# Kernel tuning notes

Measured on AMD Instinct MI355X. Metric: run time of the kernel, lower is better.

Reference implementation:

```python
import jax, jax.numpy as jnp
import numpy as np

B, S, F, DV, H, DH, L = 32, 600, 9, 1024, 16, 64, 2


def setup_inputs() -> dict:
    key = jax.random.key(0)
    ks = jax.random.split(key, 24)
    w = lambda k, shape, s=0.05: jax.random.normal(k, shape, dtype=jnp.float32) * s
    return {
        "x": w(ks[0], (B, S, F), 1.0),
        "enc_in_W": w(ks[1], (F, DV)), "enc_in_b": w(ks[2], (DV,)),
        "Wq": w(ks[3], (L, H, DV, DH)), "bq": w(ks[4], (L, H, DH)),
        "Wk": w(ks[5], (L, H, DV, DH)), "bk": w(ks[6], (L, H, DH)),
        "Wv": w(ks[7], (L, H, DV, DH)), "bv": w(ks[8], (L, H, DH)),
        "Wo": w(ks[9], (L, DV, DV)), "bo": w(ks[10], (L, DV)),
        "W1": w(ks[11], (L, DV, DV)), "b1": w(ks[12], (L, DV)),
        "W2": w(ks[13], (L, DV, DV)), "b2": w(ks[14], (L, DV)),
        "ln1_w": jnp.ones((L, DV)), "ln1_b": jnp.zeros((L, DV)),
        "ln2_w": jnp.ones((L, DV)), "ln2_b": jnp.zeros((L, DV)),
        "out_W": w(ks[15], (DV, F)), "out_b": w(ks[16], (F,)),
    }


def _layernorm(v, g, b):
    mu = v.mean(-1, keepdims=True)
    var = v.var(-1, keepdims=True)  # biased, matches torch LayerNorm
    return (v - mu) / jnp.sqrt(var + 1e-5) * g + b


def reference(x, enc_in_W, enc_in_b, Wq, bq, Wk, bk, Wv, bv, Wo, bo,
              W1, b1, W2, b2, ln1_w, ln1_b, ln2_w, ln2_b, out_W, out_b):
    # enc_input_fc; pe skipped (code checks pe_mode == 'stardard', never true)
    h = x @ enc_in_W + enc_in_b  # [B,S,DV]
    scale = 1.0 / jnp.sqrt(jnp.float32(DH))
    for l in range(L):
        q = jnp.einsum('bsd,hdk->bhsk', h, Wq[l]) + bq[l][None, :, None, :]
        k = jnp.einsum('bsd,hdk->bhsk', h, Wk[l]) + bk[l][None, :, None, :]
        v = jnp.einsum('bsd,hdk->bhsk', h, Wv[l]) + bv[l][None, :, None, :]
        attn = jax.nn.softmax(jnp.einsum('bhsk,bhtk->bhst', q, k) * scale, axis=-1)
        ctx = jnp.einsum('bhst,bhtk->bhsk', attn, v)  # [B,H,S,DH]
        # torch: stack(heads, dim=-1) -> [B,S,DH,H], then flatten(start_dim=2)
        a = ctx.transpose(0, 2, 3, 1).reshape(B, S, DH * H)
        attn_out = a @ Wo[l] + bo[l]
        x1 = _layernorm(h + attn_out, ln1_w[l], ln1_b[l])
        ff = jax.nn.elu(x1 @ W2[l] + b2[l]) @ W1[l] + b1[l]  # fc1(elu(fc2(x1)))
        h = _layernorm(x1 + ff, ln2_w[l], ln2_b[l])
    out = h @ out_W + out_b  # [B,S,F]; in_seq_len == out_seq_len -> no out_seq_fc
    return out
```

## Files before the change

### kernel.cpp

```cpp
#include <hip/hip_runtime.h>

typedef unsigned short u16;
typedef unsigned int u32;
typedef __attribute__((ext_vector_type(8))) short shortx8;
typedef __attribute__((ext_vector_type(4))) float floatx4;
typedef __attribute__((ext_vector_type(4))) u32 uintx4;
typedef __attribute__((ext_vector_type(2))) u32 uintx2;

#define AS1 __attribute__((address_space(1)))
#define AS3 __attribute__((address_space(3)))

__device__ __forceinline__ float bf2f(u16 u) {
  return __builtin_bit_cast(float, ((u32)u) << 16);
}
__device__ __forceinline__ u16 f2bf(float f) {
  u32 i = __builtin_bit_cast(u32, f);
  u32 r = (i + 0x7fffu + ((i >> 16) & 1u)) >> 16;
  return (u16)r;
}

__launch_bounds__(256)
__global__ void pack_qkv_t(const float* __restrict__ W, u16* __restrict__ dst) {
  __shared__ u16 T[64][72];
  const int kt = blockIdx.x, y = blockIdx.y;
  const int l = y >> 4, h = y & 15;
  const int t = threadIdx.x;
  const int rr = t >> 2, cq = (t & 3) * 16;
  const float* src = W + ((size_t)y * 1024 + kt * 64 + rr) * 64 + cq;
#pragma unroll
  for (int e4 = 0; e4 < 4; ++e4) {
    float4 f = *(const float4*)(src + e4 * 4);
    T[cq + e4 * 4 + 0][rr] = f2bf(f.x);
    T[cq + e4 * 4 + 1][rr] = f2bf(f.y);
    T[cq + e4 * 4 + 2][rr] = f2bf(f.z);
    T[cq + e4 * 4 + 3][rr] = f2bf(f.w);
  }
  __syncthreads();
  const int dd = t >> 2, kq = (t & 3) * 16;
  u16* drow = dst + (size_t)l * 3145728 + ((size_t)h * 64 + dd) * 1024 + kt * 64 + kq;
  *(uintx4*)(drow) = *(const uintx4*)&T[dd][kq];
  *(uintx4*)(drow + 8) = *(const uintx4*)&T[dd][kq + 8];
}

__launch_bounds__(256)
__global__ void pack_sq_t(const float* __restrict__ W, u16* __restrict__ dst) {
  __shared__ u16 T[64][72];
  const int ct = blockIdx.x & 15, rt = blockIdx.x >> 4, l = blockIdx.y;
  const int t = threadIdx.x;
  const int rr = t >> 2, cq = (t & 3) * 16;
  const float* src = W + (size_t)l * 1048576 + (size_t)(rt * 64 + rr) * 1024 + ct * 64 + cq;
#pragma unroll
  for (int e4 = 0; e4 < 4; ++e4) {
    float4 f = *(const float4*)(src + e4 * 4);
    T[cq + e4 * 4 + 0][rr] = f2bf(f.x);
    T[cq + e4 * 4 + 1][rr] = f2bf(f.y);
    T[cq + e4 * 4 + 2][rr] = f2bf(f.z);
    T[cq + e4 * 4 + 3][rr] = f2bf(f.w);
  }
  __syncthreads();
  const int cc = t >> 2, rq = (t & 3) * 16;
  u16* drow = dst + (size_t)l * 1048576 + (size_t)(ct * 64 + cc) * 1024 + rt * 64 + rq;
  *(uintx4*)(drow) = *(const uintx4*)&T[cc][rq];
  *(uintx4*)(drow + 8) = *(const uintx4*)&T[cc][rq + 8];
}

__launch_bounds__(256)
__global__ void pack_wo_t(const float* __restrict__ W, u16* __restrict__ dst) {
  __shared__ u16 T[64][72];
  const int rt = blockIdx.x >> 4, nt = blockIdx.x & 15, l = blockIdx.y;
  const int t = threadIdx.x;
  const int rr = t >> 2, cq = (t & 3) * 16;
  const float* src = W + (size_t)l * 1048576 + (size_t)(rt * 64 + rr) * 1024 + nt * 64 + cq;
#pragma unroll
  for (int e4 = 0; e4 < 4; ++e4) {
    float4 f = *(const float4*)(src + e4 * 4);
    T[cq + e4 * 4 + 0][rr] = f2bf(f.x);
    T[cq + e4 * 4 + 1][rr] = f2bf(f.y);
    T[cq + e4 * 4 + 2][rr] = f2bf(f.z);
    T[cq + e4 * 4 + 3][rr] = f2bf(f.w);
  }
  __syncthreads();
  const int hh = t & 15;
#pragma unroll
  for (int pass = 0; pass < 4; ++pass) {
    const int nl = pass * 16 + (t >> 4);
    uintx2 pk;
    u16 v0 = T[nl][0 * 16 + hh], v1 = T[nl][1 * 16 + hh];
    u16 v2 = T[nl][2 * 16 + hh], v3 = T[nl][3 * 16 + hh];
    pk[0] = (u32)v0 | ((u32)v1 << 16);
    pk[1] = (u32)v2 | ((u32)v3 << 16);
    *(uintx2*)&dst[(size_t)l * 1048576 + (size_t)(nt * 64 + nl) * 1024 + hh * 64 + rt * 4] = pk;
  }
}

__launch_bounds__(256)
__global__ void pack_bias(const float* __restrict__ bq, const float* __restrict__ bk,
                          const float* __restrict__ bv, float* __restrict__ bias) {
  const int i = blockIdx.x * 256 + threadIdx.x;
  const int l = i / 3072, n = i % 3072;
  const int which = n >> 10, nn = n & 1023;
  const float* s = (which == 0) ? bq : (which == 1) ? bk : bv;
  bias[i] = s[l * 1024 + nn];
}

__launch_bounds__(256)
__global__ void enc_kernel(const float* __restrict__ x, const float* __restrict__ W,
                           const float* __restrict__ bias, u16* __restrict__ h) {
  const size_t i = (size_t)blockIdx.x * 256 + threadIdx.x;
  const int m = (int)(i >> 10), n = (int)(i & 1023);
  const float* xr = x + (size_t)m * 9;
  float acc = bias[n];
#pragma unroll
  for (int f = 0; f < 9; ++f) acc += xr[f] * W[f * 1024 + n];
  h[i] = f2bf(acc);
}

template <int EPI>
__launch_bounds__(512)
__global__ void gemm_bt_wide(const u16* __restrict__ A, int lda,
                             const u16* __restrict__ Bt,
                             const float* __restrict__ bias,
                             const u16* __restrict__ R, int ldr,
                             u16* __restrict__ C, int ldc) {
  constexpr int K = 1024;
  __shared__ u16 As[128 * 64];
  __shared__ u16 Bs[256 * 64];
  const int tid = threadIdx.x;
  const int lane = tid & 63;
  const int w = tid >> 6;
  const int wr = w >> 2, wc = w & 3;
  const int m0 = blockIdx.y * 128, n0 = blockIdx.x * 256;

  floatx4 acc[4][4];
#pragma unroll
  for (int i = 0; i < 4; ++i)
#pragma unroll
    for (int j = 0; j < 4; ++j) acc[i][j] = (floatx4){0.f, 0.f, 0.f, 0.f};

  const u16* Ab = A + (size_t)m0 * lda;
  const u16* Bb = Bt + (size_t)n0 * K;

  for (int k0 = 0; k0 < K; k0 += 64) {
#pragma unroll
    for (int p = 0; p < 2; ++p) {
      const int o = p * 8192 + tid * 16;
      const int row = o >> 7;
      const int ke = (o & 127) >> 1;
      __builtin_amdgcn_global_load_lds((const AS1 void*)(Ab + (size_t)row * lda + (k0 + ke)),
                                       (AS3 void*)((char*)As + o), 16, 0, 0);
    }
#pragma unroll
    for (int p = 0; p < 4; ++p) {
      const int o = p * 8192 + tid * 16;
      const int row = o >> 7;
      const int ke = (o & 127) >> 1;
      __builtin_amdgcn_global_load_lds((const AS1 void*)(Bb + (size_t)row * K + (k0 + ke)),
                                       (AS3 void*)((char*)Bs + o), 16, 0, 0);
    }
    __syncthreads();
#pragma unroll
    for (int ks = 0; ks < 2; ++ks) {
      shortx8 af[4], bfr[4];
#pragma unroll
      for (int i = 0; i < 4; ++i) {
        const int ar = wr * 64 + i * 16 + (lane & 15);
        af[i] = *(const shortx8*)&As[ar * 64 + ks * 32 + (lane >> 4) * 8];
        const int br = wc * 64 + i * 16 + (lane & 15);
        bfr[i] = *(const shortx8*)&Bs[br * 64 + ks * 32 + (lane >> 4) * 8];
      }
#pragma unroll
      for (int i = 0; i < 4; ++i)
#pragma unroll
        for (int j = 0; j < 4; ++j)
          acc[i][j] = __builtin_amdgcn_mfma_f32_16x16x32_bf16(af[i], bfr[j], acc[i][j], 0, 0, 0);
    }
    __syncthreads();
  }

  const int lr = (lane >> 4) * 4, lc = lane & 15;
#pragma unroll
  for (int i = 0; i < 4; ++i) {
#pragma unroll
    for (int j = 0; j < 4; ++j) {
      const int col = n0 + wc * 64 + j * 16 + lc;
      const float bv = bias[col];
#pragma unroll
      for (int r = 0; r < 4; ++r) {
        const int row = m0 + wr * 64 + i * 16 + lr + r;
        float v = acc[i][j][r] + bv;
        if (EPI == 1) v += bf2f(R[(size_t)row * ldr + col]);
        if (EPI == 2) v = v > 0.f ? v : expm1f(v);
        C[(size_t)row * ldc + col] = f2bf(v);
      }
    }
  }
}

__launch_bounds__(256)
__global__ void attn_mfma(const u16* __restrict__ qkv, u16* __restrict__ aout) {
  const int qt = blockIdx.x, bh = blockIdx.y;
  const int b = bh >> 4, h = bh & 15;
  const int tid = threadIdx.x, lane = tid & 63, w = tid >> 6;
  const int g = lane >> 4, lq = lane & 15;

  __shared__ u16 K_ld[128 * 72];
  __shared__ u16 Vt[64 * 136];
  __shared__ u16 P_ld[4][16 * 136];

  const size_t bbase = (size_t)b * 600 * 3072;
  const int q0 = qt * 128 + w * 32;

  shortx8 aq[2][2];
#pragma unroll
  for (int sub = 0; sub < 2; ++sub) {
    const int s = q0 + sub * 16 + lq;
    if (s < 600) {
      const u16* qp = qkv + bbase + (size_t)s * 3072 + h * 64 + g * 8;
      aq[sub][0] = *(const shortx8*)qp;
      aq[sub][1] = *(const shortx8*)(qp + 32);
    } else {
      aq[sub][0] = (shortx8){0, 0, 0, 0, 0, 0, 0, 0};
      aq[sub][1] = (shortx8){0, 0, 0, 0, 0, 0, 0, 0};
    }
  }

  floatx4 Oa[2][4];
  float m[2][4], l[2][4];
#pragma unroll
  for (int sub = 0; sub < 2; ++sub) {
#pragma unroll
    for (int db = 0; db < 4; ++db) Oa[sub][db] = (floatx4){0.f, 0.f, 0.f, 0.f};
#pragma unroll
    for (int r = 0; r < 4; ++r) { m[sub][r] = -1e30f; l[sub][r] = 0.f; }
  }

  for (int ch = 0; ch < 5; ++ch) {
    const int t0 = ch * 128;
    __syncthreads();
    {
      const int tloc = tid >> 1, dhalf = (tid & 1) * 32;
      const int tg = t0 + tloc;
      if (tg < 600) {
        const u16* kp = qkv + bbase + (size_t)tg * 3072 + 1024 + h * 64 + dhalf;
        const u16* vp = kp + 1024;
#pragma unroll
        for (int c = 0; c < 4; ++c)
          *(uintx4*)&K_ld[tloc * 72 + dhalf + c * 8] = *(const uintx4*)(kp + c * 8);
#pragma unroll
        for (int c = 0; c < 4; ++c) {
          shortx8 vv = *(const shortx8*)(vp + c * 8);
#pragma unroll
          for (int e = 0; e < 8; ++e)
            Vt[(dhalf + c * 8 + e) * 136 + tloc] = (u16)vv[e];
        }
      } else {
        const uintx4 z4 = (uintx4){0, 0, 0, 0};
#pragma unroll
        for (int c = 0; c < 4; ++c)
          *(uintx4*)&K_ld[tloc * 72 + dhalf + c * 8] = z4;
#pragma unroll
        for (int c = 0; c < 4; ++c)
#pragma unroll
          for (int e = 0; e < 8; ++e)
            Vt[(dhalf + c * 8 + e) * 136 + tloc] = 0;
      }
    }
    __syncthreads();

#pragma unroll
    for (int sub = 0; sub < 2; ++sub) {
      floatx4 S[8];
      __builtin_amdgcn_s_setprio(1);
#pragma unroll
      for (int jb = 0; jb < 8; ++jb) {
        S[jb] = (floatx4){0.f, 0.f, 0.f, 0.f};
#pragma unroll
        for (int ks = 0; ks < 2; ++ks) {
          shortx8 bk = *(const shortx8*)&K_ld[(jb * 16 + lq) * 72 + ks * 32 + g * 8];
          S[jb] = __builtin_amdgcn_mfma_f32_16x16x32_bf16(aq[sub][ks], bk, S[jb], 0, 0, 0);
        }
      }
      __builtin_amdgcn_s_setprio(0);
      if (ch == 4) {
#pragma unroll
        for (int jb = 0; jb < 8; ++jb) {
          const bool ok = (t0 + jb * 16 + lq) < 600;
#pragma unroll
          for (int r = 0; r < 4; ++r) S[jb][r] = ok ? S[jb][r] * 0.125f : -1e30f;
        }
      } else {
#pragma unroll
        for (int jb = 0; jb < 8; ++jb)
#pragma unroll
          for (int r = 0; r < 4; ++r) S[jb][r] *= 0.125f;
      }

      float vmax[4];
      bool need = false;
#pragma unroll
      for (int r = 0; r < 4; ++r) {
        float v = S[0][r];
#pragma unroll
        for (int jb = 1; jb < 8; ++jb) v = fmaxf(v, S[jb][r]);
        v = fmaxf(v, __shfl_xor(v, 1));
        v = fmaxf(v, __shfl_xor(v, 2));
        v = fmaxf(v, __shfl_xor(v, 4));
        v = fmaxf(v, __shfl_xor(v, 8));
        vmax[r] = v;
        need |= (v > m[sub][r] + 8.0f);
      }
      if (__any(need ? 1 : 0)) {
#pragma unroll
        for (int r = 0; r < 4; ++r) {
          const float mn = fmaxf(m[sub][r], vmax[r]);
          const float sc = __expf(m[sub][r] - mn);
          m[sub][r] = mn;
          l[sub][r] *= sc;
#pragma unroll
          for (int db = 0; db < 4; ++db) Oa[sub][db][r] *= sc;
        }
      }

      float sums[4] = {0.f, 0.f, 0.f, 0.f};
#pragma unroll
      for (int jb = 0; jb < 8; ++jb)
#pragma unroll
        for (int r = 0; r < 4; ++r) {
          const float p = __expf(S[jb][r] - m[sub][r]);
          sums[r] += p;
          P_ld[w][(g * 4 + r) * 136 + jb * 16 + lq] = f2bf(p);
        }
#pragma unroll
      for (int r = 0; r < 4; ++r) {
        float v = sums[r];
        v += __shfl_xor(v, 1);
        v += __shfl_xor(v, 2);
        v += __shfl_xor(v, 4);
        v += __shfl_xor(v, 8);
        l[sub][r] += v;
      }

      __builtin_amdgcn_s_setprio(1);
#pragma unroll
      for (int ks = 0; ks < 4; ++ks) {
        shortx8 ap = *(const shortx8*)&P_ld[w][lq * 136 + ks * 32 + g * 8];
#pragma unroll
        for (int db = 0; db < 4; ++db) {
          shortx8 bv = *(const shortx8*)&Vt[(db * 16 + lq) * 136 + ks * 32 + g * 8];
          Oa[sub][db] = __builtin_amdgcn_mfma_f32_16x16x32_bf16(ap, bv, Oa[sub][db], 0, 0, 0);
        }
      }
      __builtin_amdgcn_s_setprio(0);
    }
  }

#pragma unroll
  for (int sub = 0; sub < 2; ++sub) {
#pragma unroll
    for (int r = 0; r < 4; ++r) {
      const int sg = q0 + sub * 16 + g * 4 + r;
      if (sg < 600) {
        const float inv = 1.f / l[sub][r];
        u16* orow = aout + ((size_t)(b * 600 + sg)) * 1024 + h * 64;
#pragma unroll
        for (int db = 0; db < 4; ++db)
          orow[db * 16 + lq] = f2bf(Oa[sub][db][r] * inv);
      }
    }
  }
}

__launch_bounds__(256)
__global__ void ln_kernel(const u16* __restrict__ y, int ldy,
                          const float* __restrict__ g, const float* __restrict__ be,
                          u16* __restrict__ o, int ldo) {
  const int row = blockIdx.x, tid = threadIdx.x;
  const int lane = tid & 63, wv = tid >> 6;
  const u16* yr = y + (size_t)row * ldy;
  const int c = tid * 4;
  const uintx2 yv = *(const uintx2*)&yr[c];
  float v0 = bf2f((u16)(yv[0] & 0xffffu)), v1 = bf2f((u16)(yv[0] >> 16));
  float v2 = bf2f((u16)(yv[1] & 0xffffu)), v3 = bf2f((u16)(yv[1] >> 16));
  float s = v0 + v1 + v2 + v3;
  float q = v0 * v0 + v1 * v1 + v2 * v2 + v3 * v3;
#pragma unroll
  for (int m = 32; m; m >>= 1) {
    s += __shfl_xor(s, m);
    q += __shfl_xor(q, m);
  }
  __shared__ float red[2][4];
  if (lane == 0) {
    red[0][wv] = s;
    red[1][wv] = q;
  }
  __syncthreads();
  s = red[0][0] + red[0][1] + red[0][2] + red[0][3];
  q = red[1][0] + red[1][1] + red[1][2] + red[1][3];
  const float mu = s * (1.f / 1024.f);
  const float var = q * (1.f / 1024.f) - mu * mu;
  const float rstd = rsqrtf(var + 1e-5f);
  const float4 gv = *(const float4*)&g[c];
  const float4 bev = *(const float4*)&be[c];
  const float o0 = (v0 - mu) * rstd * gv.x + bev.x;
  const float o1 = (v1 - mu) * rstd * gv.y + bev.y;
  const float o2 = (v2 - mu) * rstd * gv.z + bev.z;
  const float o3 = (v3 - mu) * rstd * gv.w + bev.w;
  uintx2 ov;
  ov[0] = (u32)f2bf(o0) | ((u32)f2bf(o1) << 16);
  ov[1] = (u32)f2bf(o2) | ((u32)f2bf(o3) << 16);
  *(uintx2*)&o[(size_t)row * ldo + c] = ov;
}

__launch_bounds__(256)
__global__ void out_kernel(const u16* __restrict__ h, const float* __restrict__ W,
                           const float* __restrict__ bias, float* __restrict__ out) {
  const int m = blockIdx.x * 4 + (threadIdx.x >> 6);
  const int lane = threadIdx.x & 63;
  float acc[9];
#pragma unroll
  for (int f = 0; f < 9; ++f) acc[f] = 0.f;
  const u16* hr = h + (size_t)m * 1024;
#pragma unroll 4
  for (int j = 0; j < 16; ++j) {
    const int k = lane + j * 64;
    const float hv = bf2f(hr[k]);
    const float* wr = W + (size_t)k * 9;
#pragma unroll
    for (int f = 0; f < 9; ++f) acc[f] += hv * wr[f];
  }
#pragma unroll
  for (int f = 0; f < 9; ++f)
#pragma unroll
    for (int mm = 32; mm; mm >>= 1) acc[f] += __shfl_xor(acc[f], mm);
  if (lane < 9) out[(size_t)m * 9 + lane] = acc[lane] + bias[lane];
}

extern "C" void kernel_launch(void* const* d_in, const int* in_sizes, int n_in,
                              void* d_out, int out_size, void* d_ws, size_t ws_size,
                              hipStream_t stream) {
  (void)in_sizes; (void)n_in; (void)out_size; (void)ws_size;
  const float* x     = (const float*)d_in[0];
  const float* encW  = (const float*)d_in[1];
  const float* encB  = (const float*)d_in[2];
  const float* Wq    = (const float*)d_in[3];
  const float* bq    = (const float*)d_in[4];
  const float* Wk    = (const float*)d_in[5];
  const float* bk    = (const float*)d_in[6];
  const float* Wv    = (const float*)d_in[7];
  const float* bv    = (const float*)d_in[8];
  const float* Wo    = (const float*)d_in[9];
  const float* bo    = (const float*)d_in[10];
  const float* W1    = (const float*)d_in[11];
  const float* b1    = (const float*)d_in[12];
  const float* W2    = (const float*)d_in[13];
  const float* b2    = (const float*)d_in[14];
  const float* ln1w  = (const float*)d_in[15];
  const float* ln1b  = (const float*)d_in[16];
  const float* ln2w  = (const float*)d_in[17];
  const float* ln2b  = (const float*)d_in[18];
  const float* outW  = (const float*)d_in[19];
  const float* outB  = (const float*)d_in[20];
  float* out = (float*)d_out;

  char* ws = (char*)d_ws;
  size_t off = 0;
  auto alloc = [&](size_t bytes) -> void* {
    void* p = ws + off;
    off += (bytes + 255) & ~(size_t)255;
    return p;
  };
  u16* h    = (u16*)alloc(19660800ull * 2);
  u16* qkv  = (u16*)alloc(58982400ull * 2);
  u16* abuf = (u16*)alloc(19660800ull * 2);
  u16* Bqkv = (u16*)alloc(6291456ull * 2);
  u16* Bwo  = (u16*)alloc(2097152ull * 2);
  u16* Bw1  = (u16*)alloc(2097152ull * 2);
  u16* Bw2  = (u16*)alloc(2097152ull * 2);
  float* bqkv = (float*)alloc(6144ull * 4);
  u16* ybuf = qkv;
  u16* x1   = qkv + 1024;
  u16* mid  = qkv + 2048;
  u16* y2   = abuf;

  pack_qkv_t<<<dim3(16, 32), 256, 0, stream>>>(Wq, Bqkv);
  pack_qkv_t<<<dim3(16, 32), 256, 0, stream>>>(Wk, Bqkv + 1048576);
  pack_qkv_t<<<dim3(16, 32), 256, 0, stream>>>(Wv, Bqkv + 2097152);
  pack_wo_t<<<dim3(256, 2), 256, 0, stream>>>(Wo, Bwo);
  pack_sq_t<<<dim3(256, 2), 256, 0, stream>>>(W1, Bw1);
  pack_sq_t<<<dim3(256, 2), 256, 0, stream>>>(W2, Bw2);
  pack_bias<<<24, 256, 0, stream>>>(bq, bk, bv, bqkv);
  enc_kernel<<<76800, 256, 0, stream>>>(x, encW, encB, h);

  for (int l = 0; l < 2; ++l) {
    gemm_bt_wide<0><<<dim3(12, 150), 512, 0, stream>>>(
        h, 1024, Bqkv + (size_t)l * 3145728, bqkv + l * 3072, nullptr, 0, qkv, 3072);
    attn_mfma<<<dim3(5, 512), 256, 0, stream>>>(qkv, abuf);
    gemm_bt_wide<1><<<dim3(4, 150), 512, 0, stream>>>(
        abuf, 1024, Bwo + (size_t)l * 1048576, bo + l * 1024, h, 1024, ybuf, 3072);
    ln_kernel<<<19200, 256, 0, stream>>>(ybuf, 3072, ln1w + l * 1024, ln1b + l * 1024, x1, 3072);
    gemm_bt_wide<2><<<dim3(4, 150), 512, 0, stream>>>(
        x1, 3072, Bw2 + (size_t)l * 1048576, b2 + l * 1024, nullptr, 0, mid, 3072);
    gemm_bt_wide<1><<<dim3(4, 150), 512, 0, stream>>>(
        mid, 3072, Bw1 + (size_t)l * 1048576, b1 + l * 1024, x1, 3072, y2, 1024);
    ln_kernel<<<19200, 256, 0, stream>>>(y2, 1024, ln2w + l * 1024, ln2b + l * 1024, h, 1024);
  }
  out_kernel<<<4800, 256, 0, stream>>>(h, outW, outB, out);
}
```

Before: 1.254 ms.

## Merge weight-packing kernels, vectorize encoder input, fold softmax scale into exp2

Replaces seven separate weight/bias packing launches with one kernel that dispatches on block index, which cuts launch overhead. The encoder kernel now computes eight outputs per thread and stores them as one 16-byte vector, reusing the x row loads. In attention, the 1/sqrt(d) scale is folded into an exp2 constant, so the separate scaling pass is dropped. The rescale threshold is raised to match the unscaled scores.

```diff
diff --git a/kernel.cpp b/kernel.cpp
--- a/kernel.cpp
+++ b/kernel.cpp
@@ -20,99 +20,114 @@
 }
 
 __launch_bounds__(256)
-__global__ void pack_qkv_t(const float* __restrict__ W, u16* __restrict__ dst) {
-  __shared__ u16 T[64][72];
-  const int kt = blockIdx.x, y = blockIdx.y;
-  const int l = y >> 4, h = y & 15;
+__global__ void pack_all(const float* __restrict__ Wq, const float* __restrict__ Wk,
+                         const float* __restrict__ Wv, const float* __restrict__ Wo,
+                         const float* __restrict__ W1, const float* __restrict__ W2,
+                         const float* __restrict__ bq, const float* __restrict__ bk,
+                         const float* __restrict__ bv,
+                         u16* __restrict__ Bqkv, u16* __restrict__ Bwo,
+                         u16* __restrict__ Bw1, u16* __restrict__ Bw2,
+                         float* __restrict__ bias) {
+  __shared__ u16 T[64 * 72];
+  const int blk = blockIdx.x;
   const int t = threadIdx.x;
-  const int rr = t >> 2, cq = (t & 3) * 16;
-  const float* src = W + ((size_t)y * 1024 + kt * 64 + rr) * 64 + cq;
-#pragma unroll
-  for (int e4 = 0; e4 < 4; ++e4) {
-    float4 f = *(const float4*)(src + e4 * 4);
-    T[cq + e4 * 4 + 0][rr] = f2bf(f.x);
-    T[cq + e4 * 4 + 1][rr] = f2bf(f.y);
-    T[cq + e4 * 4 + 2][rr] = f2bf(f.z);
-    T[cq + e4 * 4 + 3][rr] = f2bf(f.w);
-  }
-  __syncthreads();
-  const int dd = t >> 2, kq = (t & 3) * 16;
-  u16* drow = dst + (size_t)l * 3145728 + ((size_t)h * 64 + dd) * 1024 + kt * 64 + kq;
-  *(uintx4*)(drow) = *(const uintx4*)&T[dd][kq];
-  *(uintx4*)(drow + 8) = *(const uintx4*)&T[dd][kq + 8];
-}
-
-__launch_bounds__(256)
-__global__ void pack_sq_t(const float* __restrict__ W, u16* __restrict__ dst) {
-  __shared__ u16 T[64][72];
-  const int ct = blockIdx.x & 15, rt = blockIdx.x >> 4, l = blockIdx.y;
-  const int t = threadIdx.x;
-  const int rr = t >> 2, cq = (t & 3) * 16;
-  const float* src = W + (size_t)l * 1048576 + (size_t)(rt * 64 + rr) * 1024 + ct * 64 + cq;
-#pragma unroll
-  for (int e4 = 0; e4 < 4; ++e4) {
-    float4 f = *(const float4*)(src + e4 * 4);
-    T[cq + e4 * 4 + 0][rr] = f2bf(f.x);
-    T[cq + e4 * 4 + 1][rr] = f2bf(f.y);
-    T[cq + e4 * 4 + 2][rr] = f2bf(f.z);
-    T[cq + e4 * 4 + 3][rr] = f2bf(f.w);
-  }
-  __syncthreads();
-  const int cc = t >> 2, rq = (t & 3) * 16;
-  u16* drow = dst + (size_t)l * 1048576 + (size_t)(ct * 64 + cc) * 1024 + rt * 64 + rq;
-  *(uintx4*)(drow) = *(const uintx4*)&T[cc][rq];
-  *(uintx4*)(drow + 8) = *(const uintx4*)&T[cc][rq + 8];
-}
-
-__launch_bounds__(256)
-__global__ void pack_wo_t(const float* __restrict__ W, u16* __restrict__ dst) {
-  __shared__ u16 T[64][72];
-  const int rt = blockIdx.x >> 4, nt = blockIdx.x & 15, l = blockIdx.y;
-  const int t = threadIdx.x;
-  const int rr = t >> 2, cq = (t & 3) * 16;
-  const float* src = W + (size_t)l * 1048576 + (size_t)(rt * 64 + rr) * 1024 + nt * 64 + cq;
-#pragma unroll
-  for (int e4 = 0; e4 < 4; ++e4) {
-    float4 f = *(const float4*)(src + e4 * 4);
-    T[cq + e4 * 4 + 0][rr] = f2bf(f.x);
-    T[cq + e4 * 4 + 1][rr] = f2bf(f.y);
-    T[cq + e4 * 4 + 2][rr] = f2bf(f.z);
-    T[cq + e4 * 4 + 3][rr] = f2bf(f.w);
-  }
-  __syncthreads();
-  const int hh = t & 15;
-#pragma unroll
-  for (int pass = 0; pass < 4; ++pass) {
-    const int nl = pass * 16 + (t >> 4);
-    uintx2 pk;
-    u16 v0 = T[nl][0 * 16 + hh], v1 = T[nl][1 * 16 + hh];
-    u16 v2 = T[nl][2 * 16 + hh], v3 = T[nl][3 * 16 + hh];
-    pk[0] = (u32)v0 | ((u32)v1 << 16);
-    pk[1] = (u32)v2 | ((u32)v3 << 16);
-    *(uintx2*)&dst[(size_t)l * 1048576 + (size_t)(nt * 64 + nl) * 1024 + hh * 64 + rt * 4] = pk;
-  }
-}
-
-__launch_bounds__(256)
-__global__ void pack_bias(const float* __restrict__ bq, const float* __restrict__ bk,
-                          const float* __restrict__ bv, float* __restrict__ bias) {
-  const int i = blockIdx.x * 256 + threadIdx.x;
-  const int l = i / 3072, n = i % 3072;
-  const int which = n >> 10, nn = n & 1023;
-  const float* s = (which == 0) ? bq : (which == 1) ? bk : bv;
-  bias[i] = s[l * 1024 + nn];
+
+  if (blk < 1536) {
+    const int which = blk >> 9, r = blk & 511;
+    const int kt = r & 15, y = r >> 4;
+    const float* W = (which == 0) ? Wq : (which == 1) ? Wk : Wv;
+    u16* dst = Bqkv + (size_t)which * 1048576;
+    const int l = y >> 4, h = y & 15;
+    const int rr = t >> 2, cq = (t & 3) * 16;
+    const float* src = W + ((size_t)y * 1024 + kt * 64 + rr) * 64 + cq;
+#pragma unroll
+    for (int e4 = 0; e4 < 4; ++e4) {
+      float4 f = *(const float4*)(src + e4 * 4);
+      T[(cq + e4 * 4 + 0) * 72 + rr] = f2bf(f.x);
+      T[(cq + e4 * 4 + 1) * 72 + rr] = f2bf(f.y);
+      T[(cq + e4 * 4 + 2) * 72 + rr] = f2bf(f.z);
+      T[(cq + e4 * 4 + 3) * 72 + rr] = f2bf(f.w);
+    }
+    __syncthreads();
+    const int dd = t >> 2, kq = (t & 3) * 16;
+    u16* drow = dst + (size_t)l * 3145728 + ((size_t)h * 64 + dd) * 1024 + kt * 64 + kq;
+    *(uintx4*)(drow) = *(const uintx4*)&T[dd * 72 + kq];
+    *(uintx4*)(drow + 8) = *(const uintx4*)&T[dd * 72 + kq + 8];
+  } else if (blk < 2048) {
+    const int r = blk - 1536;
+    const int l = r >> 8, rx = r & 255;
+    const int rt = rx >> 4, nt = rx & 15;
+    const int rr = t >> 2, cq = (t & 3) * 16;
+    const float* src = Wo + (size_t)l * 1048576 + (size_t)(rt * 64 + rr) * 1024 + nt * 64 + cq;
+#pragma unroll
+    for (int e4 = 0; e4 < 4; ++e4) {
+      float4 f = *(const float4*)(src + e4 * 4);
+      T[(cq + e4 * 4 + 0) * 72 + rr] = f2bf(f.x);
+      T[(cq + e4 * 4 + 1) * 72 + rr] = f2bf(f.y);
+      T[(cq + e4 * 4 + 2) * 72 + rr] = f2bf(f.z);
+      T[(cq + e4 * 4 + 3) * 72 + rr] = f2bf(f.w);
+    }
+    __syncthreads();
+    const int hh = t & 15;
+#pragma unroll
+    for (int pass = 0; pass < 4; ++pass) {
+      const int nl = pass * 16 + (t >> 4);
+      uintx2 pk;
+      u16 v0 = T[nl * 72 + 0 * 16 + hh], v1 = T[nl * 72 + 1 * 16 + hh];
+      u16 v2 = T[nl * 72 + 2 * 16 + hh], v3 = T[nl * 72 + 3 * 16 + hh];
+      pk[0] = (u32)v0 | ((u32)v1 << 16);
+      pk[1] = (u32)v2 | ((u32)v3 << 16);
+      *(uintx2*)&Bwo[(size_t)l * 1048576 + (size_t)(nt * 64 + nl) * 1024 + hh * 64 + rt * 4] = pk;
+    }
+  } else if (blk < 3072) {
+    const int job = (blk - 2048) >> 9;
+    const int r = (blk - 2048) & 511;
+    const float* W = job == 0 ? W1 : W2;
+    u16* dst = job == 0 ? Bw1 : Bw2;
+    const int l = r >> 8, rx = r & 255;
+    const int ct = rx & 15, rt = rx >> 4;
+    const int rr = t >> 2, cq = (t & 3) * 16;
+    const float* src = W + (size_t)l * 1048576 + (size_t)(rt * 64 + rr) * 1024 + ct * 64 + cq;
+#pragma unroll
+    for (int e4 = 0; e4 < 4; ++e4) {
+      float4 f = *(const float4*)(src + e4 * 4);
+      T[(cq + e4 * 4 + 0) * 72 + rr] = f2bf(f.x);
+      T[(cq + e4 * 4 + 1) * 72 + rr] = f2bf(f.y);
+      T[(cq + e4 * 4 + 2) * 72 + rr] = f2bf(f.z);
+      T[(cq + e4 * 4 + 3) * 72 + rr] = f2bf(f.w);
+    }
+    __syncthreads();
+    const int cc = t >> 2, rq = (t & 3) * 16;
+    u16* drow = dst + (size_t)l * 1048576 + (size_t)(ct * 64 + cc) * 1024 + rt * 64 + rq;
+    *(uintx4*)(drow) = *(const uintx4*)&T[cc * 72 + rq];
+    *(uintx4*)(drow + 8) = *(const uintx4*)&T[cc * 72 + rq + 8];
+  } else {
+    const int i = (blk - 3072) * 256 + t;
+    const int l = i / 3072, n = i % 3072;
+    const int which = n >> 10, nn = n & 1023;
+    const float* s = (which == 0) ? bq : (which == 1) ? bk : bv;
+    bias[i] = s[l * 1024 + nn];
+  }
 }
 
 __launch_bounds__(256)
 __global__ void enc_kernel(const float* __restrict__ x, const float* __restrict__ W,
                            const float* __restrict__ bias, u16* __restrict__ h) {
   const size_t i = (size_t)blockIdx.x * 256 + threadIdx.x;
-  const int m = (int)(i >> 10), n = (int)(i & 1023);
+  const int m = (int)(i >> 7), nq = (int)((i & 127) << 3);
   const float* xr = x + (size_t)m * 9;
-  float acc = bias[n];
-#pragma unroll
-  for (int f = 0; f < 9; ++f) acc += xr[f] * W[f * 1024 + n];
-  h[i] = f2bf(acc);
+  float xv[9];
+#pragma unroll
+  for (int f = 0; f < 9; ++f) xv[f] = xr[f];
+  u16 ov[8];
+#pragma unroll
+  for (int e = 0; e < 8; ++e) {
+    float acc = bias[nq + e];
+#pragma unroll
+    for (int f = 0; f < 9; ++f) acc += xv[f] * W[f * 1024 + nq + e];
+    ov[e] = f2bf(acc);
+  }
+  *(uintx4*)&h[(size_t)m * 1024 + nq] = *(const uintx4*)ov;
 }
 
 template <int EPI>
@@ -202,6 +217,7 @@
   const int b = bh >> 4, h = bh & 15;
   const int tid = threadIdx.x, lane = tid & 63, w = tid >> 6;
   const int g = lane >> 4, lq = lane & 15;
+  constexpr float CE = 0.18033688011112042f;
 
   __shared__ u16 K_ld[128 * 72];
   __shared__ u16 Vt[64 * 136];
@@ -286,13 +302,8 @@
         for (int jb = 0; jb < 8; ++jb) {
           const bool ok = (t0 + jb * 16 + lq) < 600;
 #pragma unroll
-          for (int r = 0; r < 4; ++r) S[jb][r] = ok ? S[jb][r] * 0.125f : -1e30f;
+          for (int r = 0; r < 4; ++r) S[jb][r] = ok ? S[jb][r] : -1e30f;
         }
-      } else {
-#pragma unroll
-        for (int jb = 0; jb < 8; ++jb)
-#pragma unroll
-          for (int r = 0; r < 4; ++r) S[jb][r] *= 0.125f;
       }
 
       float vmax[4];
@@ -307,13 +318,13 @@
         v = fmaxf(v, __shfl_xor(v, 4));
         v = fmaxf(v, __shfl_xor(v, 8));
         vmax[r] = v;
-        need |= (v > m[sub][r] + 8.0f);
+        need |= (v > m[sub][r] + 64.0f);
       }
       if (__any(need ? 1 : 0)) {
 #pragma unroll
         for (int r = 0; r < 4; ++r) {
           const float mn = fmaxf(m[sub][r], vmax[r]);
-          const float sc = __expf(m[sub][r] - mn);
+          const float sc = exp2f((m[sub][r] - mn) * CE);
           m[sub][r] = mn;
           l[sub][r] *= sc;
 #pragma unroll
@@ -326,7 +337,7 @@
       for (int jb = 0; jb < 8; ++jb)
 #pragma unroll
         for (int r = 0; r < 4; ++r) {
-          const float p = __expf(S[jb][r] - m[sub][r]);
+          const float p = exp2f((S[jb][r] - m[sub][r]) * CE);
           sums[r] += p;
           P_ld[w][(g * 4 + r) * 136 + jb * 16 + lq] = f2bf(p);
         }
@@ -482,14 +493,9 @@
   u16* mid  = qkv + 2048;
   u16* y2   = abuf;
 
-  pack_qkv_t<<<dim3(16, 32), 256, 0, stream>>>(Wq, Bqkv);
-  pack_qkv_t<<<dim3(16, 32), 256, 0, stream>>>(Wk, Bqkv + 1048576);
-  pack_qkv_t<<<dim3(16, 32), 256, 0, stream>>>(Wv, Bqkv + 2097152);
-  pack_wo_t<<<dim3(256, 2), 256, 0, stream>>>(Wo, Bwo);
-  pack_sq_t<<<dim3(256, 2), 256, 0, stream>>>(W1, Bw1);
-  pack_sq_t<<<dim3(256, 2), 256, 0, stream>>>(W2, Bw2);
-  pack_bias<<<24, 256, 0, stream>>>(bq, bk, bv, bqkv);
-  enc_kernel<<<76800, 256, 0, stream>>>(x, encW, encB, h);
+  pack_all<<<3096, 256, 0, stream>>>(Wq, Wk, Wv, Wo, W1, W2, bq, bk, bv,
+                                     Bqkv, Bwo, Bw1, Bw2, bqkv);
+  enc_kernel<<<9600, 256, 0, stream>>>(x, encW, encB, h);
 
   for (int l = 0; l < 2; ++l) {
     gemm_bt_wide<0><<<dim3(12, 150), 512, 0, stream>>>(
```

Result: no change. 1.275 ms (+1.7%).
